# Kernel optimization log

Measured on AMD Instinct MI355X. Metric: run time of the kernel, lower is better.

The kernel has to match this reference:

```python
import jax, jax.numpy as jnp
import numpy as np

T, H, I, E, K = 2048, 2048, 1408, 8, 2


def setup_inputs() -> dict:
    key = jax.random.key(0)
    k1, k2, k3, k4, k5 = jax.random.split(key, 5)
    s_h = 1.0 / np.sqrt(H)
    s_i = 1.0 / np.sqrt(I)
    return {
        "hidden_states": jax.random.normal(k1, (T, H), dtype=jnp.float32),
        "router_logits": jax.random.normal(k2, (T, E), dtype=jnp.float32),
        "Wg": jax.random.normal(k3, (E, H, I), dtype=jnp.float32) * s_h,
        "Wu": jax.random.normal(k4, (E, H, I), dtype=jnp.float32) * s_h,
        "Wd": jax.random.normal(k5, (E, I, H), dtype=jnp.float32) * s_i,
        "top_k": K,
    }


def reference(hidden_states, router_logits, Wg, Wu, Wd, top_k):
    # top-k routing: softmax over the selected top-k logits (as in torch.topk + softmax)
    topk_vals, topk_ids = jax.lax.top_k(router_logits, top_k)  # [T,K]
    topk_w = jax.nn.softmax(topk_vals, axis=-1)                # [T,K]

    n_tok = hidden_states.shape[0]
    n_exp = router_logits.shape[-1]
    # combine weights [T,E]: scatter top-k weights back to expert slots
    cw = jnp.zeros((n_tok, n_exp), hidden_states.dtype)
    cw = cw.at[jnp.arange(n_tok)[:, None], topk_ids].add(topk_w)

    out = jnp.zeros_like(hidden_states)
    for e in range(n_exp):  # small fixed expert count
        g = hidden_states @ Wg[e]          # [T,I]
        u = hidden_states @ Wu[e]          # [T,I]
        y = (jax.nn.silu(g) * u) @ Wd[e]   # [T,H]
        out = out + cw[:, e:e + 1] * y
    return out
```

## Files before the change

kernel.cpp:

```cpp
#include <hip/hip_runtime.h>
#include <hip/hip_bf16.h>
#include <cstdint>
#include <cstddef>

#define TT 2048
#define HH 2048
#define II 1408
#define EE 8
#define MAXROWS 5120

typedef unsigned short u16;
typedef __attribute__((ext_vector_type(8))) __bf16 bf16x8;
typedef __attribute__((ext_vector_type(4))) float f32x4;

typedef const __attribute__((address_space(1))) uint32_t* gas1_t;
typedef __attribute__((address_space(3))) uint32_t* las3_t;

#define VM_WAIT(N) asm volatile("s_waitcnt vmcnt(" #N ")" ::: "memory")
#define IR_FENCE() asm volatile("" ::: "memory")

__device__ __forceinline__ float bf2f(u16 b) {
    return __uint_as_float(((uint32_t)b) << 16);
}
__device__ __forceinline__ u16 f2bf(float x) {
    uint32_t u = __float_as_uint(x);
    u += 0x7fffu + ((u >> 16) & 1u);
    return (u16)(u >> 16);
}

__global__ void k_sniff(const u16* __restrict__ raw, int* __restrict__ flag,
                        int* __restrict__ counts) {
    __shared__ int cnt;
    if (threadIdx.x < EE) counts[threadIdx.x] = 0;
    if (threadIdx.x == 0) cnt = 0;
    __syncthreads();
    int w = 0;
    for (int i = threadIdx.x; i < 4096; i += 256) {
        u16 x = raw[i];
        if (x & 0x7fff) {
            int ex = (x >> 7) & 0xff;
            if (ex == 0xff || ex < 100 || ex > 140) ++w;
        }
    }
    atomicAdd(&cnt, w);
    __syncthreads();
    if (threadIdx.x == 0) flag[0] = (cnt > 100) ? 1 : 0;
}

__global__ void k_routing2(const void* __restrict__ logits, const int* __restrict__ flag,
                           int* __restrict__ counts, int* __restrict__ idx,
                           float* __restrict__ wt, int* __restrict__ slot) {
    int t = blockIdx.x * 256 + threadIdx.x;
    if (t >= TT) return;
    const int f = flag[0];
    float v[EE];
#pragma unroll
    for (int e = 0; e < EE; ++e)
        v[e] = f ? ((const float*)logits)[t * EE + e]
                 : bf2f(((const u16*)logits)[t * EE + e]);
    int i0 = 0; float v0 = v[0];
#pragma unroll
    for (int e = 1; e < EE; ++e) { if (v[e] > v0) { v0 = v[e]; i0 = e; } }
    int i1 = -1; float v1 = -3.4e38f;
#pragma unroll
    for (int e = 0; e < EE; ++e) { if (e != i0 && v[e] > v1) { v1 = v[e]; i1 = e; } }
    float r = __expf(v1 - v0);
    float s = 1.f / (1.f + r);
    int p0 = atomicAdd(&counts[i0], 1);
    idx[i0 * TT + p0] = t; wt[i0 * TT + p0] = s;
    slot[t * 2 + 0] = i0 * TT + p0;
    int p1 = atomicAdd(&counts[i1], 1);
    idx[i1 * TT + p1] = t; wt[i1 * TT + p1] = r * s;
    slot[t * 2 + 1] = i1 * TT + p1;
}

__global__ void k_offsets(const int* __restrict__ counts, int* __restrict__ meta) {
    if (threadIdx.x == 0 && blockIdx.x == 0) {
        int off = 0;
        for (int e = 0; e < EE; ++e) {
            int c = counts[e];
            int p = (c + 127) & ~127;
            meta[e] = off; meta[8 + e] = p;
            off += p;
        }
    }
}

__global__ void k_cast(const void* __restrict__ src, const int* __restrict__ flag,
                       u16* __restrict__ dst) {
    const int i0 = (blockIdx.x * 256 + threadIdx.x) * 8;
    if (flag[0]) {
        const float* s = (const float*)src;
#pragma unroll
        for (int j = 0; j < 8; ++j) dst[i0 + j] = f2bf(s[i0 + j]);
    } else {
        const u16* s = (const u16*)src;
        *(uint4*)&dst[i0] = *(const uint4*)&s[i0];
    }
}

__global__ void k_transposeV(const void* __restrict__ src, const int* __restrict__ flag,
                             u16* __restrict__ dst, int R, int C) {
    __shared__ u16 t[64][68];
    const size_t eo = (size_t)blockIdx.z * (size_t)R * (size_t)C;
    const int r0 = blockIdx.y * 64, c0 = blockIdx.x * 64;
    const int tid = threadIdx.x;
    const int f = flag[0];
    {
        const int cg = tid & 15, rr = tid >> 4;
#pragma unroll
        for (int p = 0; p < 4; ++p) {
            const int r = rr + p * 16;
            const size_t base = eo + (size_t)(r0 + r) * C + c0 + cg * 4;
            if (f) {
                const float4 v = *(const float4*)((const float*)src + base);
                t[r][cg * 4 + 0] = f2bf(v.x); t[r][cg * 4 + 1] = f2bf(v.y);
                t[r][cg * 4 + 2] = f2bf(v.z); t[r][cg * 4 + 3] = f2bf(v.w);
            } else {
                const ushort4 v = *(const ushort4*)((const u16*)src + base);
                t[r][cg * 4 + 0] = v.x; t[r][cg * 4 + 1] = v.y;
                t[r][cg * 4 + 2] = v.z; t[r][cg * 4 + 3] = v.w;
            }
        }
    }
    __syncthreads();
    {
        const int rg = tid & 15, cc = tid >> 4;
#pragma unroll
        for (int p = 0; p < 4; ++p) {
            const int c = cc + p * 16;
            ushort4 o;
            o.x = t[rg * 4 + 0][c]; o.y = t[rg * 4 + 1][c];
            o.z = t[rg * 4 + 2][c]; o.w = t[rg * 4 + 3][c];
            *(ushort4*)(dst + eo + (size_t)(c0 + c) * R + r0 + rg * 4) = o;
        }
    }
}


#define G1_COMPUTE(B) do { \
    __builtin_amdgcn_s_setprio(1); \
    bf16x8 af[4]; \
    _Pragma("unroll") \
    for (int mi = 0; mi < 4; ++mi) \
        af[mi] = *(const bf16x8*)&As[B][(wr + mi * 16 + ln) * 32 + qx]; \
    _Pragma("unroll") \
    for (int ni = 0; ni < 2; ++ni) { \
        bf16x8 bgf = *(const bf16x8*)&Bg[B][(wc + ni * 16 + ln) * 32 + qx]; \
        bf16x8 buf_ = *(const bf16x8*)&Bu[B][(wc + ni * 16 + ln) * 32 + qx]; \
        _Pragma("unroll") \
        for (int mi = 0; mi < 4; ++mi) { \
            accg[mi][ni] = __builtin_amdgcn_mfma_f32_16x16x32_bf16(af[mi], bgf, accg[mi][ni], 0, 0, 0); \
            accu[mi][ni] = __builtin_amdgcn_mfma_f32_16x16x32_bf16(af[mi], buf_, accu[mi][ni], 0, 0, 0); \
        } \
    } \
    __builtin_amdgcn_s_setprio(0); \
} while (0)

#define G1_STAGE(B, KB) do { \
    __builtin_amdgcn_global_load_lds((gas1_t)(pA + (KB)), (las3_t)(&As[B][dofs]), 16, 0, 0); \
    __builtin_amdgcn_global_load_lds((gas1_t)(pG + (KB)), (las3_t)(&Bg[B][dofs]), 16, 0, 0); \
    __builtin_amdgcn_global_load_lds((gas1_t)(pU + (KB)), (las3_t)(&Bu[B][dofs]), 16, 0, 0); \
} while (0)

__global__ __launch_bounds__(512, 4)
void k_gemm1s(const u16* __restrict__ hs_b,
              const u16* __restrict__ Wgt,
              const u16* __restrict__ Wut,
              const int* __restrict__ counts,
              const int* __restrict__ meta,
              const int* __restrict__ idx,
              const float* __restrict__ wt,
              u16* __restrict__ act_g) {
    const int e = blockIdx.x;
    const int cnt = counts[e];
    const int pcnt = meta[8 + e];
    const int m0 = blockIdx.y * 128;
    if (m0 >= pcnt) return;
    const int n0 = blockIdx.z * 128;
    const int off = meta[e];
    const int tid = threadIdx.x;
    const int wave = tid >> 6, lane = tid & 63;
    const int ln = lane & 15, q = lane >> 4;
    const int wr = (wave >> 2) * 64;
    const int wc = (wave & 3) * 32;

    __shared__ __align__(16) u16 As[3][128 * 32];
    __shared__ __align__(16) u16 Bg[3][128 * 32];
    __shared__ __align__(16) u16 Bu[3][128 * 32];
    __shared__ int   tokS[128];
    __shared__ float wtS[128];

    if (tid < 128) {
        const int pos = m0 + tid;
        const bool v = pos < cnt;
        tokS[tid] = v ? idx[e * TT + pos] : 0;
        wtS[tid]  = v ? wt[e * TT + pos] : 0.f;
    }
    __syncthreads();

    const int srow = tid >> 2;
    const int csw  = (((tid & 3) ^ ((srow >> 1) & 3))) * 8;
    const u16* pA = hs_b + (size_t)tokS[srow] * HH + csw;
    const u16* pG = Wgt + ((size_t)e * II + n0 + srow) * HH + csw;
    const u16* pU = Wut + ((size_t)e * II + n0 + srow) * HH + csw;
    const int dofs = tid * 8;

    const int qx = (q ^ ((ln >> 1) & 3)) * 8;

    f32x4 accg[4][2], accu[4][2];
#pragma unroll
    for (int mi = 0; mi < 4; ++mi)
#pragma unroll
        for (int ni = 0; ni < 2; ++ni) { accg[mi][ni] = (f32x4)0.f; accu[mi][ni] = (f32x4)0.f; }

    G1_STAGE(0, 0);
    G1_STAGE(1, 32);
    int b0 = 0, b1 = 1, b2 = 2;
    for (int t = 0; t < 62; ++t) {
        G1_STAGE(b2, (t + 2) * 32);
        VM_WAIT(6);
        __builtin_amdgcn_s_barrier();
        G1_COMPUTE(b0);
        IR_FENCE();
        __builtin_amdgcn_s_barrier();
        const int tb = b0; b0 = b1; b1 = b2; b2 = tb;
    }
    VM_WAIT(3);
    __builtin_amdgcn_s_barrier();
    G1_COMPUTE(b0);
    VM_WAIT(0);
    __builtin_amdgcn_s_barrier();
    G1_COMPUTE(b1);

#pragma unroll
    for (int mi = 0; mi < 4; ++mi) {
#pragma unroll
        for (int r = 0; r < 4; ++r) {
            const int row = wr + mi * 16 + q * 4 + r;
            const float w = wtS[row];
#pragma unroll
            for (int ni = 0; ni < 2; ++ni) {
                const int i = n0 + wc + ni * 16 + ln;
                const float g = accg[mi][ni][r];
                const float u = accu[mi][ni][r];
                const float y = w * u * g / (1.f + __expf(-g));
                act_g[(size_t)(off + m0 + row) * II + i] = f2bf(y);
            }
        }
    }
}

#define G2_COMPUTE(B) do { \
    __builtin_amdgcn_s_setprio(1); \
    bf16x8 af[4]; \
    _Pragma("unroll") \
    for (int mi = 0; mi < 4; ++mi) \
        af[mi] = *(const bf16x8*)&As[B][(wr + mi * 16 + ln) * 32 + qx]; \
    _Pragma("unroll") \
    for (int ni = 0; ni < 4; ++ni) { \
        bf16x8 bf = *(const bf16x8*)&Bs[B][(wc + ni * 16 + ln) * 32 + qx]; \
        _Pragma("unroll") \
        for (int mi = 0; mi < 4; ++mi) \
            acc[mi][ni] = __builtin_amdgcn_mfma_f32_16x16x32_bf16(af[mi], bf, acc[mi][ni], 0, 0, 0); \
    } \
    __builtin_amdgcn_s_setprio(0); \
} while (0)

#define G2_STAGE(B, KB) do { \
    __builtin_amdgcn_global_load_lds((gas1_t)(pA0 + (KB)), (las3_t)(&As[B][dofs]), 16, 0, 0); \
    __builtin_amdgcn_global_load_lds((gas1_t)(pA1 + (KB)), (las3_t)(&As[B][2048 + dofs]), 16, 0, 0); \
    __builtin_amdgcn_global_load_lds((gas1_t)(pB0 + (KB)), (las3_t)(&Bs[B][dofs]), 16, 0, 0); \
    __builtin_amdgcn_global_load_lds((gas1_t)(pB1 + (KB)), (las3_t)(&Bs[B][2048 + dofs]), 16, 0, 0); \
} while (0)

__global__ __launch_bounds__(256, 3)
void k_gemm2s(const u16* __restrict__ act_g,
              const u16* __restrict__ Wdt,
              const int* __restrict__ meta,
              float* __restrict__ y_g) {
    const int e = blockIdx.x;
    const int pcnt = meta[8 + e];
    const int m0 = blockIdx.y * 128;
    if (m0 >= pcnt) return;
    const int n0 = blockIdx.z * 128;
    const int off = meta[e];
    const int tid = threadIdx.x;
    const int wave = tid >> 6, lane = tid & 63;
    const int ln = lane & 15, q = lane >> 4;
    const int wr = (wave >> 1) * 64, wc = (wave & 1) * 64;

    __shared__ __align__(16) u16 As[3][128 * 32];
    __shared__ __align__(16) u16 Bs[3][128 * 32];

    const int srow = tid >> 2;
    const int csw  = (((tid & 3) ^ ((srow >> 1) & 3))) * 8;
    const u16* bA = act_g + (size_t)(off + m0) * II;
    const u16* bB = Wdt + ((size_t)e * HH + n0) * II;
    const u16* pA0 = bA + (size_t)srow * II + csw;
    const u16* pA1 = bA + (size_t)(srow + 64) * II + csw;
    const u16* pB0 = bB + (size_t)srow * II + csw;
    const u16* pB1 = bB + (size_t)(srow + 64) * II + csw;
    const int dofs = tid * 8;

    const int qx = (q ^ ((ln >> 1) & 3)) * 8;

    f32x4 acc[4][4];
#pragma unroll
    for (int mi = 0; mi < 4; ++mi)
#pragma unroll
        for (int ni = 0; ni < 4; ++ni) acc[mi][ni] = (f32x4)0.f;

    G2_STAGE(0, 0);
    G2_STAGE(1, 32);
    int b0 = 0, b1 = 1, b2 = 2;
    for (int t = 0; t < 42; ++t) {
        G2_STAGE(b2, (t + 2) * 32);
        VM_WAIT(8);
        __builtin_amdgcn_s_barrier();
        G2_COMPUTE(b0);
        IR_FENCE();
        __builtin_amdgcn_s_barrier();
        const int tb = b0; b0 = b1; b1 = b2; b2 = tb;
    }
    VM_WAIT(4);
    __builtin_amdgcn_s_barrier();
    G2_COMPUTE(b0);
    VM_WAIT(0);
    __builtin_amdgcn_s_barrier();
    G2_COMPUTE(b1);

#pragma unroll
    for (int mi = 0; mi < 4; ++mi) {
#pragma unroll
        for (int r = 0; r < 4; ++r) {
            const int row = wr + mi * 16 + q * 4 + r;
            float* dst = y_g + (size_t)(off + m0 + row) * HH + n0 + wc;
#pragma unroll
            for (int ni = 0; ni < 4; ++ni)
                dst[ni * 16 + ln] = acc[mi][ni][r];
        }
    }
}

__global__ void k_combine(const float* __restrict__ y_g, const int* __restrict__ slot,
                          const int* __restrict__ meta, const int* __restrict__ flag,
                          void* __restrict__ out) {
    const int gid = blockIdx.x * 256 + threadIdx.x;
    const int t = gid >> 9;
    const int h = (gid & 511) * 4;
    const int s0 = slot[t * 2 + 0], s1 = slot[t * 2 + 1];
    const int r0 = meta[s0 >> 11] + (s0 & 2047);
    const int r1 = meta[s1 >> 11] + (s1 & 2047);
    const float4 a = *(const float4*)&y_g[(size_t)r0 * HH + h];
    const float4 b = *(const float4*)&y_g[(size_t)r1 * HH + h];
    const float4 v = make_float4(a.x + b.x, a.y + b.y, a.z + b.z, a.w + b.w);
    if (flag[0]) {
        *(float4*)((float*)out + (size_t)t * HH + h) = v;
    } else {
        u16* o = (u16*)out + (size_t)t * HH + h;
        o[0] = f2bf(v.x); o[1] = f2bf(v.y); o[2] = f2bf(v.z); o[3] = f2bf(v.w);
    }
}

extern "C" void kernel_launch(void* const* d_in, const int* in_sizes, int n_in,
                              void* d_out, int out_size, void* d_ws, size_t ws_size,
                              hipStream_t stream) {
    (void)in_sizes; (void)n_in; (void)out_size;
    const void* hs     = d_in[0];
    const void* logits = d_in[1];
    const void* Wg     = d_in[2];
    const void* Wu     = d_in[3];
    const void* Wd     = d_in[4];

    char* ws = (char*)d_ws;
    size_t off = 0;
    int*   flag   = (int*)(ws + off);   off += 256;
    int*   counts = (int*)(ws + off);   off += 256;
    int*   meta   = (int*)(ws + off);   off += 256;
    int*   idx    = (int*)(ws + off);   off += (size_t)EE * TT * 4;
    float* wt     = (float*)(ws + off); off += (size_t)EE * TT * 4;
    int*   slot   = (int*)(ws + off);   off += (size_t)TT * 2 * 4;
    u16*   hs_b   = (u16*)(ws + off);   off += (size_t)TT * HH * 2;
    u16*   Wgt    = (u16*)(ws + off);   off += (size_t)EE * II * HH * 2;
    u16*   Wut    = (u16*)(ws + off);   off += (size_t)EE * II * HH * 2;
    u16*   Wdt    = (u16*)(ws + off);   off += (size_t)EE * HH * II * 2;
    u16*   act_g  = (u16*)(ws + off);   off += (size_t)MAXROWS * II * 2;
    float* y_g    = (float*)(ws + off); off += (size_t)MAXROWS * HH * 4;
    if (ws_size < off) return;

    k_sniff<<<dim3(1), dim3(256), 0, stream>>>((const u16*)hs, flag, counts);
    k_routing2<<<dim3(TT / 256), dim3(256), 0, stream>>>(logits, flag, counts, idx, wt, slot);
    k_offsets<<<dim3(1), dim3(64), 0, stream>>>(counts, meta);
    k_cast<<<dim3(TT * HH / (256 * 8)), dim3(256), 0, stream>>>(hs, flag, hs_b);
    k_transposeV<<<dim3(II / 64, HH / 64, EE), dim3(256), 0, stream>>>(Wg, flag, Wgt, HH, II);
    k_transposeV<<<dim3(II / 64, HH / 64, EE), dim3(256), 0, stream>>>(Wu, flag, Wut, HH, II);
    k_transposeV<<<dim3(HH / 64, II / 64, EE), dim3(256), 0, stream>>>(Wd, flag, Wdt, II, HH);
    k_gemm1s<<<dim3(EE, TT / 128, II / 128), dim3(512), 0, stream>>>(hs_b, Wgt, Wut, counts, meta, idx, wt, act_g);
    k_gemm2s<<<dim3(EE, TT / 128, HH / 128), dim3(256), 0, stream>>>(act_g, Wdt, meta, y_g);
    k_combine<<<dim3(TT * HH / (256 * 4)), dim3(256), 0, stream>>>(y_g, slot, meta, flag, d_out);
}
```

Before: 526.3 us.

## Shrink GEMM tiles to 128x64 and 64x128, rewrite weight transpose with packed stores

The weight transpose kernel now packs two adjacent rows into 32-bit words in shared memory and writes 16-byte vectors, replacing the 8-byte scattered stores. GEMM1 moves from 512-thread 128x128 tiles to 256-thread 128x64 tiles. GEMM2 moves from 128x128 tiles to 64x128 tiles. Together these raise the block count and occupancy for the ragged per-expert matrices, at the cost of less reuse per tile and more redundant loads of A or B.

Measured after the change: 562.5 us. 6.9% more time.

```diff
diff --git a/kernel.cpp b/kernel.cpp
--- a/kernel.cpp
+++ b/kernel.cpp
@@ -99,42 +99,53 @@
     }
 }
 
-__global__ void k_transposeV(const void* __restrict__ src, const int* __restrict__ flag,
+__global__ void k_transposeP(const void* __restrict__ src, const int* __restrict__ flag,
                              u16* __restrict__ dst, int R, int C) {
-    __shared__ u16 t[64][68];
+    __shared__ uint32_t TTs[64 * 34];
     const size_t eo = (size_t)blockIdx.z * (size_t)R * (size_t)C;
     const int r0 = blockIdx.y * 64, c0 = blockIdx.x * 64;
     const int tid = threadIdx.x;
     const int f = flag[0];
-    {
-        const int cg = tid & 15, rr = tid >> 4;
-#pragma unroll
-        for (int p = 0; p < 4; ++p) {
-            const int r = rr + p * 16;
-            const size_t base = eo + (size_t)(r0 + r) * C + c0 + cg * 4;
-            if (f) {
-                const float4 v = *(const float4*)((const float*)src + base);
-                t[r][cg * 4 + 0] = f2bf(v.x); t[r][cg * 4 + 1] = f2bf(v.y);
-                t[r][cg * 4 + 2] = f2bf(v.z); t[r][cg * 4 + 3] = f2bf(v.w);
-            } else {
-                const ushort4 v = *(const ushort4*)((const u16*)src + base);
-                t[r][cg * 4 + 0] = v.x; t[r][cg * 4 + 1] = v.y;
-                t[r][cg * 4 + 2] = v.z; t[r][cg * 4 + 3] = v.w;
-            }
+    const int cg = (tid & 15) * 4;
+    const int rh = tid >> 4;
+#pragma unroll
+    for (int p = 0; p < 2; ++p) {
+        const int rp = rh + 16 * p;
+        const int r  = 2 * rp;
+        const size_t base = eo + (size_t)(r0 + r) * C + c0 + cg;
+        uint32_t w0, w1, w2, w3;
+        if (f) {
+            const float4 v0 = *(const float4*)((const float*)src + base);
+            const float4 v1 = *(const float4*)((const float*)src + base + C);
+            w0 = (uint32_t)f2bf(v0.x) | ((uint32_t)f2bf(v1.x) << 16);
+            w1 = (uint32_t)f2bf(v0.y) | ((uint32_t)f2bf(v1.y) << 16);
+            w2 = (uint32_t)f2bf(v0.z) | ((uint32_t)f2bf(v1.z) << 16);
+            w3 = (uint32_t)f2bf(v0.w) | ((uint32_t)f2bf(v1.w) << 16);
+        } else {
+            const ushort4 v0 = *(const ushort4*)((const u16*)src + base);
+            const ushort4 v1 = *(const ushort4*)((const u16*)src + base + C);
+            w0 = (uint32_t)v0.x | ((uint32_t)v1.x << 16);
+            w1 = (uint32_t)v0.y | ((uint32_t)v1.y << 16);
+            w2 = (uint32_t)v0.z | ((uint32_t)v1.z << 16);
+            w3 = (uint32_t)v0.w | ((uint32_t)v1.w << 16);
         }
+        TTs[(cg + 0) * 34 + rp] = w0;
+        TTs[(cg + 1) * 34 + rp] = w1;
+        TTs[(cg + 2) * 34 + rp] = w2;
+        TTs[(cg + 3) * 34 + rp] = w3;
     }
     __syncthreads();
-    {
-        const int rg = tid & 15, cc = tid >> 4;
-#pragma unroll
-        for (int p = 0; p < 4; ++p) {
-            const int c = cc + p * 16;
-            ushort4 o;
-            o.x = t[rg * 4 + 0][c]; o.y = t[rg * 4 + 1][c];
-            o.z = t[rg * 4 + 2][c]; o.w = t[rg * 4 + 3][c];
-            *(ushort4*)(dst + eo + (size_t)(c0 + c) * R + r0 + rg * 4) = o;
-        }
-    }
+    const int c = tid >> 2, u = tid & 3;
+    uint32_t o[8];
+#pragma unroll
+    for (int k = 0; k < 4; ++k) {
+        const int rp = 8 * u + 2 * k;
+        o[2 * k]     = TTs[c * 34 + rp];
+        o[2 * k + 1] = TTs[c * 34 + rp + 1];
+    }
+    u16* dp = dst + eo + (size_t)(c0 + c) * R + r0 + 16 * u;
+    *(uint4*)(dp)     = make_uint4(o[0], o[1], o[2], o[3]);
+    *(uint4*)(dp + 8) = make_uint4(o[4], o[5], o[6], o[7]);
 }
 
 
@@ -158,12 +169,13 @@
 } while (0)
 
 #define G1_STAGE(B, KB) do { \
-    __builtin_amdgcn_global_load_lds((gas1_t)(pA + (KB)), (las3_t)(&As[B][dofs]), 16, 0, 0); \
+    __builtin_amdgcn_global_load_lds((gas1_t)(pA0 + (KB)), (las3_t)(&As[B][dofs]), 16, 0, 0); \
+    __builtin_amdgcn_global_load_lds((gas1_t)(pA1 + (KB)), (las3_t)(&As[B][2048 + dofs]), 16, 0, 0); \
     __builtin_amdgcn_global_load_lds((gas1_t)(pG + (KB)), (las3_t)(&Bg[B][dofs]), 16, 0, 0); \
     __builtin_amdgcn_global_load_lds((gas1_t)(pU + (KB)), (las3_t)(&Bu[B][dofs]), 16, 0, 0); \
 } while (0)
 
-__global__ __launch_bounds__(512, 4)
+__global__ __launch_bounds__(256, 4)
 void k_gemm1s(const u16* __restrict__ hs_b,
               const u16* __restrict__ Wgt,
               const u16* __restrict__ Wut,
@@ -177,17 +189,17 @@
     const int pcnt = meta[8 + e];
     const int m0 = blockIdx.y * 128;
     if (m0 >= pcnt) return;
-    const int n0 = blockIdx.z * 128;
+    const int n0 = blockIdx.z * 64;
     const int off = meta[e];
     const int tid = threadIdx.x;
     const int wave = tid >> 6, lane = tid & 63;
     const int ln = lane & 15, q = lane >> 4;
-    const int wr = (wave >> 2) * 64;
-    const int wc = (wave & 3) * 32;
+    const int wr = (wave >> 1) * 64;
+    const int wc = (wave & 1) * 32;
 
     __shared__ __align__(16) u16 As[3][128 * 32];
-    __shared__ __align__(16) u16 Bg[3][128 * 32];
-    __shared__ __align__(16) u16 Bu[3][128 * 32];
+    __shared__ __align__(16) u16 Bg[3][64 * 32];
+    __shared__ __align__(16) u16 Bu[3][64 * 32];
     __shared__ int   tokS[128];
     __shared__ float wtS[128];
 
@@ -201,7 +213,8 @@
 
     const int srow = tid >> 2;
     const int csw  = (((tid & 3) ^ ((srow >> 1) & 3))) * 8;
-    const u16* pA = hs_b + (size_t)tokS[srow] * HH + csw;
+    const u16* pA0 = hs_b + (size_t)tokS[srow] * HH + csw;
+    const u16* pA1 = hs_b + (size_t)tokS[srow + 64] * HH + csw;
     const u16* pG = Wgt + ((size_t)e * II + n0 + srow) * HH + csw;
     const u16* pU = Wut + ((size_t)e * II + n0 + srow) * HH + csw;
     const int dofs = tid * 8;
@@ -219,14 +232,14 @@
     int b0 = 0, b1 = 1, b2 = 2;
     for (int t = 0; t < 62; ++t) {
         G1_STAGE(b2, (t + 2) * 32);
-        VM_WAIT(6);
+        VM_WAIT(8);
         __builtin_amdgcn_s_barrier();
         G1_COMPUTE(b0);
         IR_FENCE();
         __builtin_amdgcn_s_barrier();
         const int tb = b0; b0 = b1; b1 = b2; b2 = tb;
     }
-    VM_WAIT(3);
+    VM_WAIT(4);
     __builtin_amdgcn_s_barrier();
     G1_COMPUTE(b0);
     VM_WAIT(0);
@@ -256,10 +269,10 @@
     bf16x8 af[4]; \
     _Pragma("unroll") \
     for (int mi = 0; mi < 4; ++mi) \
-        af[mi] = *(const bf16x8*)&As[B][(wr + mi * 16 + ln) * 32 + qx]; \
+        af[mi] = *(const bf16x8*)&As[B][(mi * 16 + ln) * 32 + qx]; \
     _Pragma("unroll") \
-    for (int ni = 0; ni < 4; ++ni) { \
-        bf16x8 bf = *(const bf16x8*)&Bs[B][(wc + ni * 16 + ln) * 32 + qx]; \
+    for (int ni = 0; ni < 2; ++ni) { \
+        bf16x8 bf = *(const bf16x8*)&Bs[B][(wc2 + ni * 16 + ln) * 32 + qx]; \
         _Pragma("unroll") \
         for (int mi = 0; mi < 4; ++mi) \
             acc[mi][ni] = __builtin_amdgcn_mfma_f32_16x16x32_bf16(af[mi], bf, acc[mi][ni], 0, 0, 0); \
@@ -268,62 +281,58 @@
 } while (0)
 
 #define G2_STAGE(B, KB) do { \
-    __builtin_amdgcn_global_load_lds((gas1_t)(pA0 + (KB)), (las3_t)(&As[B][dofs]), 16, 0, 0); \
-    __builtin_amdgcn_global_load_lds((gas1_t)(pA1 + (KB)), (las3_t)(&As[B][2048 + dofs]), 16, 0, 0); \
+    __builtin_amdgcn_global_load_lds((gas1_t)(pA + (KB)), (las3_t)(&As[B][dofs]), 16, 0, 0); \
     __builtin_amdgcn_global_load_lds((gas1_t)(pB0 + (KB)), (las3_t)(&Bs[B][dofs]), 16, 0, 0); \
     __builtin_amdgcn_global_load_lds((gas1_t)(pB1 + (KB)), (las3_t)(&Bs[B][2048 + dofs]), 16, 0, 0); \
 } while (0)
 
-__global__ __launch_bounds__(256, 3)
+__global__ __launch_bounds__(256, 4)
 void k_gemm2s(const u16* __restrict__ act_g,
               const u16* __restrict__ Wdt,
               const int* __restrict__ meta,
               float* __restrict__ y_g) {
     const int e = blockIdx.x;
     const int pcnt = meta[8 + e];
-    const int m0 = blockIdx.y * 128;
+    const int m0 = blockIdx.y * 64;
     if (m0 >= pcnt) return;
     const int n0 = blockIdx.z * 128;
     const int off = meta[e];
     const int tid = threadIdx.x;
     const int wave = tid >> 6, lane = tid & 63;
     const int ln = lane & 15, q = lane >> 4;
-    const int wr = (wave >> 1) * 64, wc = (wave & 1) * 64;
-
-    __shared__ __align__(16) u16 As[3][128 * 32];
+    const int wc2 = wave * 32;
+
+    __shared__ __align__(16) u16 As[3][64 * 32];
     __shared__ __align__(16) u16 Bs[3][128 * 32];
 
     const int srow = tid >> 2;
     const int csw  = (((tid & 3) ^ ((srow >> 1) & 3))) * 8;
-    const u16* bA = act_g + (size_t)(off + m0) * II;
-    const u16* bB = Wdt + ((size_t)e * HH + n0) * II;
-    const u16* pA0 = bA + (size_t)srow * II + csw;
-    const u16* pA1 = bA + (size_t)(srow + 64) * II + csw;
-    const u16* pB0 = bB + (size_t)srow * II + csw;
-    const u16* pB1 = bB + (size_t)(srow + 64) * II + csw;
+    const u16* pA  = act_g + (size_t)(off + m0 + srow) * II + csw;
+    const u16* pB0 = Wdt + ((size_t)e * HH + n0 + srow) * II + csw;
+    const u16* pB1 = Wdt + ((size_t)e * HH + n0 + srow + 64) * II + csw;
     const int dofs = tid * 8;
 
     const int qx = (q ^ ((ln >> 1) & 3)) * 8;
 
-    f32x4 acc[4][4];
+    f32x4 acc[4][2];
 #pragma unroll
     for (int mi = 0; mi < 4; ++mi)
 #pragma unroll
-        for (int ni = 0; ni < 4; ++ni) acc[mi][ni] = (f32x4)0.f;
+        for (int ni = 0; ni < 2; ++ni) acc[mi][ni] = (f32x4)0.f;
 
     G2_STAGE(0, 0);
     G2_STAGE(1, 32);
     int b0 = 0, b1 = 1, b2 = 2;
     for (int t = 0; t < 42; ++t) {
         G2_STAGE(b2, (t + 2) * 32);
-        VM_WAIT(8);
+        VM_WAIT(6);
         __builtin_amdgcn_s_barrier();
         G2_COMPUTE(b0);
         IR_FENCE();
         __builtin_amdgcn_s_barrier();
         const int tb = b0; b0 = b1; b1 = b2; b2 = tb;
     }
-    VM_WAIT(4);
+    VM_WAIT(3);
     __builtin_amdgcn_s_barrier();
     G2_COMPUTE(b0);
     VM_WAIT(0);
@@ -334,10 +343,10 @@
     for (int mi = 0; mi < 4; ++mi) {
 #pragma unroll
         for (int r = 0; r < 4; ++r) {
-            const int row = wr + mi * 16 + q * 4 + r;
-            float* dst = y_g + (size_t)(off + m0 + row) * HH + n0 + wc;
-#pragma unroll
-            for (int ni = 0; ni < 4; ++ni)
+            const int row = mi * 16 + q * 4 + r;
+            float* dst = y_g + (size_t)(off + m0 + row) * HH + n0 + wc2;
+#pragma unroll
+            for (int ni = 0; ni < 2; ++ni)
                 dst[ni * 16 + ln] = acc[mi][ni][r];
         }
     }
@@ -393,10 +402,10 @@
     k_routing2<<<dim3(TT / 256), dim3(256), 0, stream>>>(logits, flag, counts, idx, wt, slot);
     k_offsets<<<dim3(1), dim3(64), 0, stream>>>(counts, meta);
     k_cast<<<dim3(TT * HH / (256 * 8)), dim3(256), 0, stream>>>(hs, flag, hs_b);
-    k_transposeV<<<dim3(II / 64, HH / 64, EE), dim3(256), 0, stream>>>(Wg, flag, Wgt, HH, II);
-    k_transposeV<<<dim3(II / 64, HH / 64, EE), dim3(256), 0, stream>>>(Wu, flag, Wut, HH, II);
-    k_transposeV<<<dim3(HH / 64, II / 64, EE), dim3(256), 0, stream>>>(Wd, flag, Wdt, II, HH);
-    k_gemm1s<<<dim3(EE, TT / 128, II / 128), dim3(512), 0, stream>>>(hs_b, Wgt, Wut, counts, meta, idx, wt, act_g);
-    k_gemm2s<<<dim3(EE, TT / 128, HH / 128), dim3(256), 0, stream>>>(act_g, Wdt, meta, y_g);
+    k_transposeP<<<dim3(II / 64, HH / 64, EE), dim3(256), 0, stream>>>(Wg, flag, Wgt, HH, II);
+    k_transposeP<<<dim3(II / 64, HH / 64, EE), dim3(256), 0, stream>>>(Wu, flag, Wut, HH, II);
+    k_transposeP<<<dim3(HH / 64, II / 64, EE), dim3(256), 0, stream>>>(Wd, flag, Wdt, II, HH);
+    k_gemm1s<<<dim3(EE, TT / 128, II / 64), dim3(256), 0, stream>>>(hs_b, Wgt, Wut, counts, meta, idx, wt, act_g);
+    k_gemm2s<<<dim3(EE, TT / 64, HH / 128), dim3(256), 0, stream>>>(act_g, Wdt, meta, y_g);
     k_combine<<<dim3(TT * HH / (256 * 4)), dim3(256), 0, stream>>>(y_g, slot, meta, flag, d_out);
 }
```
